# Kernel tuning notes

Hardware: AMD Instinct MI355X
Metric: run time of the kernel (lower is better)

Reference implementation:

```python
import jax, jax.numpy as jnp
import numpy as np

B = 65536      # batch size
H = 256        # hidden_size (args['hid_dim'])
MID = 300      # hard-coded encoder bottleneck in CommonFeatureExtractor
THR = 0.6      # similarity_threshold


def _lin(k, fin, fout):
    return jax.random.normal(k, (fin, fout), jnp.float32) / np.sqrt(fin)


def setup_inputs() -> dict:
    key = jax.random.key(0)
    ks = jax.random.split(key, 24)
    inp = {
        'brics': jax.random.normal(ks[0], (B, H), jnp.float32),
        'function_group': jax.random.normal(ks[1], (B, H), jnp.float32),
        'pharmacophore': jax.random.normal(ks[2], (B, H), jnp.float32),
    }
    # three fp encoders: Linear(H,300) -> ReLU -> (Dropout eval) -> Linear(300,H)
    for n, (k1, k2) in zip(['b', 'f', 'p'], [(ks[3], ks[4]), (ks[5], ks[6]), (ks[7], ks[8])]):
        inp['W1_' + n] = _lin(k1, H, MID)
        inp['b1_' + n] = jnp.zeros((MID,), jnp.float32)
        inp['W2_' + n] = _lin(k2, MID, H)
        inp['b2_' + n] = jnp.zeros((H,), jnp.float32)
    inp['Wg'] = _lin(ks[9], 3 * H, 3)        # weight_generator
    inp['bg_v'] = jnp.zeros((3,), jnp.float32)
    inp['We'] = _lin(ks[10], H, H)           # enhancement_layer
    inp['be_v'] = jnp.zeros((H,), jnp.float32)
    inp['Wf'] = _lin(ks[11], 2 * H, H)       # fusion_layer
    inp['bf_v'] = jnp.zeros((H,), jnp.float32)
    return inp


def _fwd(brics, function_group, pharmacophore,
         W1_b, b1_b, W2_b, b2_b, W1_f, b1_f, W2_f, b2_f, W1_p, b1_p, W2_p, b2_p,
         Wg, bg_v, We, be_v, Wf, bf_v):
    def enc(x, W1, b1, W2, b2):
        return jax.nn.relu(x @ W1 + b1) @ W2 + b2  # dropout in eval mode = identity

    eb = enc(brics, W1_b, b1_b, W2_b, b2_b)
    ef = enc(function_group, W1_f, b1_f, W2_f, b2_f)
    ep = enc(pharmacophore, W1_p, b1_p, W2_p, b2_p)

    fps = jnp.stack([eb, ef, ep], axis=1)                              # [B,3,H]
    fpn = fps / jnp.maximum(jnp.linalg.norm(fps, axis=-1, keepdims=True), 1e-12)

    # the 3 unordered pairs (0,1),(0,2),(1,2); the torch sort is irrelevant
    # because the selected pairs are combined by a permutation-invariant
    # softmax-weighted sum.
    ii = jnp.array([0, 0, 1])
    jj = jnp.array([1, 2, 2])
    elem = fpn[:, ii] * fpn[:, jj]                                     # [B,3,H]
    sims = elem.sum(-1)                                                # [B,3] cosine sims
    pmask = sims > THR
    common = 0.5 * (fps[:, ii] + fps[:, jj]) * (elem > THR)            # [B,3,H]

    has = pmask.any(-1)                                                # [B]
    m = jnp.max(jnp.where(pmask, sims, -jnp.inf), axis=-1, keepdims=True)
    m = jnp.where(jnp.isfinite(m), m, 0.0)
    e = jnp.where(pmask, jnp.exp(sims - m), 0.0)                       # masked softmax
    w = e / jnp.maximum(e.sum(-1, keepdims=True), 1e-12)
    sample_common = (common * w[..., None]).sum(1)                     # [B,H]
    common_features = jnp.where(has[:, None], sample_common, fps.mean(1))

    allc = jnp.concatenate([eb, ef, ep], axis=1)                       # [B,3H]
    fw = jax.nn.softmax(allc @ Wg + bg_v, axis=1)                      # [B,3]
    weighted = eb * fw[:, 0:1] + ef * fw[:, 1:2] + ep * fw[:, 2:3]

    enh = jax.nn.sigmoid(common_features @ We + be_v)
    fused = jnp.concatenate([weighted, common_features * enh], axis=1) @ Wf + bf_v
    return fused


def reference(brics, function_group, pharmacophore,
              W1_b, b1_b, W2_b, b2_b, W1_f, b1_f, W2_f, b2_f, W1_p, b1_p, W2_p, b2_p,
              Wg, bg_v, We, be_v, Wf, bf_v):
    return _fwd(brics, function_group, pharmacophore,
                W1_b, b1_b, W2_b, b2_b, W1_f, b1_f, W2_f, b2_f, W1_p, b1_p, W2_p, b2_p,
                Wg, bg_v, We, be_v, Wf, bf_v)
```

## Files before the change

### kernel.cpp

```cpp
#include <hip/hip_runtime.h>

typedef unsigned short u16;
typedef __bf16 bf16x8 __attribute__((ext_vector_type(8)));
typedef float f32x4 __attribute__((ext_vector_type(4)));
typedef unsigned short u16x8 __attribute__((ext_vector_type(8)));

__device__ __forceinline__ float b2f(u16 b){ union{unsigned u; float f;} v; v.u=((unsigned)b)<<16; return v.f; }
__device__ __forceinline__ u16 f2b(float f){ unsigned u=__builtin_bit_cast(unsigned,f); return (u16)((u+0x7fffu+((u>>16)&1u))>>16); }
__device__ __forceinline__ float wred32(float v){
  #pragma unroll
  for(int off=16; off>0; off>>=1) v += __shfl_xor(v, off, 64);
  return v;
}

__device__ __forceinline__ void gload_lds16(const void* g, void* l){
  __builtin_amdgcn_global_load_lds(
      (const __attribute__((address_space(1))) void*)g,
      (__attribute__((address_space(3))) void*)l, 16, 0, 0);
}

template<int PER>
__device__ __forceinline__ void stage_tile_b16(const u16* __restrict__ base, int rstride,
                                               int kcol, u16* lds, int w, int lane){
  #pragma unroll
  for(int it=0; it<PER; ++it){
    int cbase = it*512 + w*64;
    int ch = cbase + lane;
    int r = ch >> 3;
    int ce = ((ch & 7) * 8) ^ ((r & 7) << 3);
    gload_lds16(base + (size_t)r*rstride + kcol + ce, lds + cbase*8);
  }
}

struct Af32Regs { float4 a0, b0, a1, b1; };
__device__ __forceinline__ void loadA_f32(Af32Regs& rg, const float* __restrict__ Ap,
                                          int lda, int kcol, int tid){
  {
    int ch = tid;       int r = ch>>3, s = (ch&7)*8;
    const float* src = Ap + (size_t)r*lda + kcol + s;
    rg.a0 = *(const float4*)src; rg.b0 = *(const float4*)(src+4);
  }
  {
    int ch = tid + 512; int r = ch>>3, s = (ch&7)*8;
    const float* src = Ap + (size_t)r*lda + kcol + s;
    rg.a1 = *(const float4*)src; rg.b1 = *(const float4*)(src+4);
  }
}
__device__ __forceinline__ void writeA_f32(const Af32Regs& rg, u16* As, int tid){
  {
    int ch = tid;       int r = ch>>3, s = (ch&7)*8;
    u16* dst = &As[r*64 + (s ^ ((r&7)<<3))];
    ushort4 o0{f2b(rg.a0.x),f2b(rg.a0.y),f2b(rg.a0.z),f2b(rg.a0.w)};
    ushort4 o1{f2b(rg.b0.x),f2b(rg.b0.y),f2b(rg.b0.z),f2b(rg.b0.w)};
    *(ushort4*)dst = o0; *(ushort4*)(dst+4) = o1;
  }
  {
    int ch = tid + 512; int r = ch>>3, s = (ch&7)*8;
    u16* dst = &As[r*64 + (s ^ ((r&7)<<3))];
    ushort4 o0{f2b(rg.a1.x),f2b(rg.a1.y),f2b(rg.a1.z),f2b(rg.a1.w)};
    ushort4 o1{f2b(rg.b1.x),f2b(rg.b1.y),f2b(rg.b1.z),f2b(rg.b1.w)};
    *(ushort4*)dst = o0; *(ushort4*)(dst+4) = o1;
  }
}

struct GP {
  const void* A[3];
  const u16*  Wt[3];
  const float* bias[3];
  void* C[3];
  int lda, K, Nreal, ldc;
};

template<int MODE, typename AT, int NWT>
__global__ __launch_bounds__(512, 2) void gemm_w(GP p)
{
  constexpr int BN = NWT*64;
  constexpr int AHALF = 128*64;
  constexpr int BHALF = BN*64;
  __shared__ __align__(16) u16 smem[2*AHALF + 2*BHALF];

  const int z = blockIdx.z;
  const AT* __restrict__ A  = (const AT*)p.A[z];
  const u16* __restrict__ Wt = p.Wt[z];
  const float* __restrict__ bias = p.bias[z];
  u16* __restrict__ C = (u16*)p.C[z];
  const int lda = p.lda, K = p.K, ldc = p.ldc;

  const int tid = threadIdx.x;
  const size_t m0 = (size_t)blockIdx.x * 128;
  const int lane = tid & 63, w = tid >> 6;
  const int lr = lane & 15, quad = lane >> 4;
  const int wr = (w >> 2) * 64, wc = (w & 3) * (NWT*16);
  const int swz = (lr & 7) << 3;
  const int NT = K >> 6;

  f32x4 acc[4][NWT];
  #pragma unroll
  for(int i=0;i<4;++i)
    #pragma unroll
    for(int j=0;j<NWT;++j) acc[i][j] = (f32x4){0.f,0.f,0.f,0.f};

  const AT* Ab = A + m0*(size_t)lda;

  if constexpr (__is_same(AT, u16)) {
    stage_tile_b16<2>((const u16*)Ab, lda, 0, smem, w, lane);
  } else {
    Af32Regs rg; loadA_f32(rg, (const float*)Ab, lda, 0, tid);
    writeA_f32(rg, smem, tid);
  }
  stage_tile_b16<NWT>(Wt, K, 0, smem + 2*AHALF, w, lane);
  __syncthreads();

  int cur = 0;
  for(int t=0; t<NT; ++t){
    const int knext = (t+1) << 6;
    const bool pf = (t+1) < NT;
    Af32Regs rg;
    if (pf){
      if constexpr (__is_same(AT, u16))
        stage_tile_b16<2>((const u16*)Ab, lda, knext, smem + (cur^1)*AHALF, w, lane);
      else
        loadA_f32(rg, (const float*)Ab, lda, knext, tid);
      stage_tile_b16<NWT>(Wt, K, knext, smem + 2*AHALF + (cur^1)*BHALF, w, lane);
    }
    const u16* Asc = smem + cur*AHALF;
    const u16* Bsc = smem + 2*AHALF + cur*BHALF;
    #pragma unroll
    for(int kk=0; kk<64; kk+=32){
      bf16x8 af[4], bq[NWT];
      #pragma unroll
      for(int i=0;i<4;++i)
        af[i] = *(const bf16x8*)&Asc[(wr + i*16 + lr)*64 + ((kk + quad*8) ^ swz)];
      #pragma unroll
      for(int j=0;j<NWT;++j)
        bq[j] = *(const bf16x8*)&Bsc[(wc + j*16 + lr)*64 + ((kk + quad*8) ^ swz)];
      #pragma unroll
      for(int i=0;i<4;++i)
        #pragma unroll
        for(int j=0;j<NWT;++j)
          acc[i][j] = __builtin_amdgcn_mfma_f32_16x16x32_bf16(af[i], bq[j], acc[i][j], 0, 0, 0);
    }
    if constexpr (!__is_same(AT, u16)) { if (pf) writeA_f32(rg, smem + (cur^1)*AHALF, tid); }
    __syncthreads();
    cur ^= 1;
  }

  constexpr int BNP = BN + 8;
  static_assert(128*BNP <= 2*AHALF + 2*BHALF, "Ct fits in smem");
  u16* Ct = smem;
  #pragma unroll
  for(int j=0;j<NWT;++j){
    int col = wc + j*16 + lr;
    float bv = (col < p.Nreal) ? bias[col] : 0.f;
    #pragma unroll
    for(int i=0;i<4;++i){
      #pragma unroll
      for(int r=0;r<4;++r){
        float v = acc[i][j][r] + bv;
        if(MODE==1) v = fmaxf(v, 0.f);
        Ct[(wr + i*16 + quad*4 + r)*BNP + col] = f2b(v);
      }
    }
  }
  __syncthreads();
  const int rowg = tid >> 2, cg = tid & 3;
  const size_t crow = (m0 + rowg)*(size_t)ldc;
  #pragma unroll
  for(int k2=0; k2<BN/32; ++k2){
    int c = (cg + k2*4)*8;
    *(u16x8*)&C[crow + c] = *(const u16x8*)&Ct[rowg*BNP + c];
  }
}

struct TPar { const float* src; u16* dst; int K, N, Kp, Np; };
struct TArgs { TPar p[8]; };
__global__ __launch_bounds__(256) void transpose_all(TArgs args){
  TPar p = args.p[blockIdx.y];
  int n = blockIdx.x;
  if (n >= p.Np) return;
  for (int k = threadIdx.x; k < p.Kp; k += 256){
    u16 v = 0;
    if (n < p.N && k < p.K) v = f2b(p.src[(size_t)k*p.N + n]);
    p.dst[(size_t)n*p.Kp + k] = v;
  }
}

__global__ __launch_bounds__(512, 2) void fuse3_k(
    const u16* __restrict__ eb, const u16* __restrict__ ef, const u16* __restrict__ ep,
    const float* __restrict__ Wg, const float* __restrict__ bg,
    const u16* __restrict__ WtE, const float* __restrict__ be,
    const u16* __restrict__ WtF, const float* __restrict__ bfv,
    float* __restrict__ out)
{
  constexpr int BHALF = 256*64;
  __shared__ __align__(16) u16 cw[4*64*64];
  __shared__ __align__(16) u16 ww[4*64*64];
  __shared__ __align__(16) u16 Bst[2*BHALF];

  const int tid = threadIdx.x;
  const size_t m0 = (size_t)blockIdx.x * 64;
  const int lane = tid & 63, w = tid >> 6;
  const int lr = lane & 15, quad = lane >> 4;
  const int wr = (w >> 2) * 32, wc = (w & 3) * 64;
  const int swz = (lr & 7) << 3;

  stage_tile_b16<4>(WtE, 256, 0, Bst, w, lane);

  const int rid = tid >> 5, l5 = tid & 31;
  for(int pass=0; pass<4; ++pass){
    int rloc = pass*16 + rid;
    size_t base = (m0 + rloc)*256 + l5*8;

    u16x8 vb = *(const u16x8*)(eb + base);
    u16x8 vf = *(const u16x8*)(ef + base);
    u16x8 vp = *(const u16x8*)(ep + base);
    float fb[8], ff[8], fp[8];
    #pragma unroll
    for(int j=0;j<8;++j){ fb[j]=b2f(vb[j]); ff[j]=b2f(vf[j]); fp[j]=b2f(vp[j]); }

    float sb=0, sf=0, sp=0, d01=0, d02=0, d12=0, g0=0, g1=0, g2=0;
    #pragma unroll
    for(int j=0;j<8;++j){
      sb += fb[j]*fb[j]; sf += ff[j]*ff[j]; sp += fp[j]*fp[j];
      d01 += fb[j]*ff[j]; d02 += fb[j]*fp[j]; d12 += ff[j]*fp[j];
    }
    #pragma unroll
    for(int seg=0; seg<3; ++seg){
      const float* x = (seg==0) ? fb : (seg==1) ? ff : fp;
      const float* wg = Wg + ((size_t)seg*256 + l5*8)*3;
      float wv[24];
      #pragma unroll
      for(int q=0;q<6;++q){
        float4 t = *(const float4*)(wg + q*4);
        wv[q*4+0]=t.x; wv[q*4+1]=t.y; wv[q*4+2]=t.z; wv[q*4+3]=t.w;
      }
      #pragma unroll
      for(int j=0;j<8;++j){
        g0 += x[j]*wv[j*3+0];
        g1 += x[j]*wv[j*3+1];
        g2 += x[j]*wv[j*3+2];
      }
    }
    sb=wred32(sb); sf=wred32(sf); sp=wred32(sp);
    d01=wred32(d01); d02=wred32(d02); d12=wred32(d12);
    g0=wred32(g0); g1=wred32(g1); g2=wred32(g2);

    float inb  = __builtin_amdgcn_rsqf(fmaxf(sb, 1e-24f));
    float invf = __builtin_amdgcn_rsqf(fmaxf(sf, 1e-24f));
    float inp  = __builtin_amdgcn_rsqf(fmaxf(sp, 1e-24f));
    float s01 = d01*inb*invf, s02 = d02*inb*inp, s12 = d12*invf*inp;

    float h0 = g0 + bg[0], h1 = g1 + bg[1], h2 = g2 + bg[2];
    float gm = fmaxf(h0, fmaxf(h1, h2));
    float e0 = __expf(h0-gm), e1 = __expf(h1-gm), e2 = __expf(h2-gm);
    float res = __builtin_amdgcn_rcpf(e0+e1+e2);
    float fw0 = e0*res, fw1 = e1*res, fw2 = e2*res;

    bool p0 = s01 > 0.6f, p1 = s02 > 0.6f, p2 = s12 > 0.6f;
    bool has = p0 || p1 || p2;
    float mm = -__builtin_inff();
    if(p0) mm = fmaxf(mm, s01);
    if(p1) mm = fmaxf(mm, s02);
    if(p2) mm = fmaxf(mm, s12);
    if(!has) mm = 0.f;
    float q0 = p0 ? __expf(s01-mm) : 0.f;
    float q1 = p1 ? __expf(s02-mm) : 0.f;
    float q2 = p2 ? __expf(s12-mm) : 0.f;
    float rqs = __builtin_amdgcn_rcpf(fmaxf(q0+q1+q2, 1e-12f));
    float w0 = q0*rqs, w1 = q1*rqs, w2 = q2*rqs;

    u16x8 oc, ow;
    #pragma unroll
    for(int j=0;j<8;++j){
      float a = fb[j], b = ff[j], c = fp[j];
      float na = a*inb, nbv = b*invf, nc = c*inp;
      float c0 = (na*nbv > 0.6f) ? 0.5f*(a+b) : 0.f;
      float c1 = (na*nc  > 0.6f) ? 0.5f*(a+c) : 0.f;
      float c2 = (nbv*nc > 0.6f) ? 0.5f*(b+c) : 0.f;
      float sc = c0*w0 + c1*w1 + c2*w2;
      float cf = has ? sc : (a+b+c)*(1.f/3.f);
      float wv = a*fw0 + b*fw1 + c*fw2;
      oc[j] = f2b(cf); ow[j] = f2b(wv);
    }
    int idx = (l5>>3)*4096 + rloc*64 + (((l5&7)*8) ^ ((rloc&7)<<3));
    *(u16x8*)&cw[idx] = oc;
    *(u16x8*)&ww[idx] = ow;
  }
  __syncthreads();

  f32x4 ga[2][4];
  #pragma unroll
  for(int i=0;i<2;++i)
    #pragma unroll
    for(int j=0;j<4;++j) ga[i][j] = (f32x4){0.f,0.f,0.f,0.f};

  int cur = 0;
  for(int t=0; t<4; ++t){
    if(t<3) stage_tile_b16<4>(WtE, 256, (t+1)*64, Bst + (cur^1)*BHALF, w, lane);
    const u16* Asc = cw + t*4096;
    const u16* Bsc = Bst + cur*BHALF;
    #pragma unroll
    for(int kk=0; kk<64; kk+=32){
      bf16x8 af[2], bq[4];
      #pragma unroll
      for(int i=0;i<2;++i)
        af[i] = *(const bf16x8*)&Asc[(wr + i*16 + lr)*64 + ((kk + quad*8) ^ swz)];
      #pragma unroll
      for(int j=0;j<4;++j)
        bq[j] = *(const bf16x8*)&Bsc[(wc + j*16 + lr)*64 + ((kk + quad*8) ^ swz)];
      #pragma unroll
      for(int i=0;i<2;++i)
        #pragma unroll
        for(int j=0;j<4;++j)
          ga[i][j] = __builtin_amdgcn_mfma_f32_16x16x32_bf16(af[i], bq[j], ga[i][j], 0, 0, 0);
    }
    __syncthreads();
    cur ^= 1;
  }
  stage_tile_b16<4>(WtF, 512, 0, Bst, w, lane);

  #pragma unroll
  for(int j=0;j<4;++j){
    int col = wc + j*16 + lr;
    float bev = be[col];
    int within = j*16 + lr;
    #pragma unroll
    for(int i=0;i<2;++i){
      #pragma unroll
      for(int r=0;r<4;++r){
        int rl = wr + i*16 + quad*4 + r;
        int idx = (w & 3)*4096 + rl*64 + (within ^ ((rl&7)<<3));
        float cv = b2f(cw[idx]);
        float v = ga[i][j][r] + bev;
        cw[idx] = f2b(cv * __builtin_amdgcn_rcpf(1.f + __expf(-v)));
      }
    }
  }
  __syncthreads();

  f32x4 fa[2][4];
  #pragma unroll
  for(int i=0;i<2;++i)
    #pragma unroll
    for(int j=0;j<4;++j) fa[i][j] = (f32x4){0.f,0.f,0.f,0.f};

  cur = 0;
  for(int t=0; t<8; ++t){
    if(t<7) stage_tile_b16<4>(WtF, 512, (t+1)*64, Bst + (cur^1)*BHALF, w, lane);
    const u16* Asc = (t < 4) ? (ww + t*4096) : (cw + (t-4)*4096);
    const u16* Bsc = Bst + cur*BHALF;
    #pragma unroll
    for(int kk=0; kk<64; kk+=32){
      bf16x8 af[2], bq[4];
      #pragma unroll
      for(int i=0;i<2;++i)
        af[i] = *(const bf16x8*)&Asc[(wr + i*16 + lr)*64 + ((kk + quad*8) ^ swz)];
      #pragma unroll
      for(int j=0;j<4;++j)
        bq[j] = *(const bf16x8*)&Bsc[(wc + j*16 + lr)*64 + ((kk + quad*8) ^ swz)];
      #pragma unroll
      for(int i=0;i<2;++i)
        #pragma unroll
        for(int j=0;j<4;++j)
          fa[i][j] = __builtin_amdgcn_mfma_f32_16x16x32_bf16(af[i], bq[j], fa[i][j], 0, 0, 0);
    }
    __syncthreads();
    cur ^= 1;
  }

  #pragma unroll
  for(int j=0;j<4;++j){
    int col = wc + j*16 + lr;
    float bfc = bfv[col];
    #pragma unroll
    for(int i=0;i<2;++i){
      #pragma unroll
      for(int r=0;r<4;++r){
        size_t row = m0 + wr + i*16 + quad*4 + r;
        out[row*256 + col] = fa[i][j][r] + bfc;
      }
    }
  }
}

extern "C" void kernel_launch(void* const* d_in, const int* in_sizes, int n_in,
                              void* d_out, int out_size, void* d_ws, size_t ws_size,
                              hipStream_t stream) {
  const float* brics = (const float*)d_in[0];
  const float* fg    = (const float*)d_in[1];
  const float* ph    = (const float*)d_in[2];
  const float* W1[3] = {(const float*)d_in[3], (const float*)d_in[7], (const float*)d_in[11]};
  const float* b1[3] = {(const float*)d_in[4], (const float*)d_in[8], (const float*)d_in[12]};
  const float* W2[3] = {(const float*)d_in[5], (const float*)d_in[9], (const float*)d_in[13]};
  const float* b2[3] = {(const float*)d_in[6], (const float*)d_in[10], (const float*)d_in[14]};
  const float* Wg = (const float*)d_in[15];
  const float* bg = (const float*)d_in[16];
  const float* We = (const float*)d_in[17];
  const float* be = (const float*)d_in[18];
  const float* Wf = (const float*)d_in[19];
  const float* bf = (const float*)d_in[20];
  float* out = (float*)d_out;

  const int M = in_sizes[0] / 256;

  char* wsp = (char*)d_ws;
  size_t off = 0;
  auto carve = [&](size_t elems)->u16* {
    u16* p = (u16*)(wsp + off);
    off += ((elems*sizeof(u16)) + 255) & ~(size_t)255;
    return p;
  };
  u16* xb0 = carve((size_t)M*256);
  u16* xb1 = carve((size_t)M*256);
  u16* xb2 = carve((size_t)M*256);
  u16* Wt1[3], *Wt2[3];
  for(int i=0;i<3;++i) Wt1[i] = carve(320*256);
  for(int i=0;i<3;++i) Wt2[i] = carve(256*320);
  u16* WtE = carve(256*256);
  u16* WtF = carve(256*512);

  size_t hb = (((size_t)M*320*sizeof(u16)) + 255) & ~(size_t)255;
  bool batched = (off + 3*hb) <= ws_size;
  u16* hh[3];
  hh[0] = (u16*)(wsp + off);
  hh[1] = batched ? (u16*)(wsp + off + hb)   : hh[0];
  hh[2] = batched ? (u16*)(wsp + off + 2*hb) : hh[0];
  (void)n_in; (void)out_size;

  TArgs ta;
  for(int i=0;i<3;++i){
    ta.p[i]   = {W1[i], Wt1[i], 256, 300, 256, 320};
    ta.p[3+i] = {W2[i], Wt2[i], 300, 256, 320, 256};
  }
  ta.p[6] = {We, WtE, 256, 256, 256, 256};
  ta.p[7] = {Wf, WtF, 512, 256, 512, 256};
  transpose_all<<<dim3(512, 8), 256, 0, stream>>>(ta);

  const float* xin[3] = {brics, fg, ph};
  u16* encp[3] = {xb0, xb1, xb2};
  if (batched) {
    GP g1{};
    for(int i=0;i<3;++i){ g1.A[i]=xin[i]; g1.Wt[i]=Wt1[i]; g1.bias[i]=b1[i]; g1.C[i]=hh[i]; }
    g1.lda=256; g1.K=256; g1.Nreal=300; g1.ldc=320;
    gemm_w<1,float,5><<<dim3(M/128, 1, 3), 512, 0, stream>>>(g1);
    GP g2{};
    for(int i=0;i<3;++i){ g2.A[i]=hh[i]; g2.Wt[i]=Wt2[i]; g2.bias[i]=b2[i]; g2.C[i]=encp[i]; }
    g2.lda=320; g2.K=320; g2.Nreal=256; g2.ldc=256;
    gemm_w<0,u16,4><<<dim3(M/128, 1, 3), 512, 0, stream>>>(g2);
  } else {
    for(int i=0;i<3;++i){
      GP g1{}; g1.A[0]=xin[i]; g1.Wt[0]=Wt1[i]; g1.bias[0]=b1[i]; g1.C[0]=hh[0];
      g1.lda=256; g1.K=256; g1.Nreal=300; g1.ldc=320;
      gemm_w<1,float,5><<<dim3(M/128, 1, 1), 512, 0, stream>>>(g1);
      GP g2{}; g2.A[0]=hh[0]; g2.Wt[0]=Wt2[i]; g2.bias[0]=b2[i]; g2.C[0]=encp[i];
      g2.lda=320; g2.K=320; g2.Nreal=256; g2.ldc=256;
      gemm_w<0,u16,4><<<dim3(M/128, 1, 1), 512, 0, stream>>>(g2);
    }
  }

  fuse3_k<<<M/64, 512, 0, stream>>>(xb0, xb1, xb2, Wg, bg, WtE, be, WtF, bf, out);
}
```

Measured before the change: 434.4 us.

## Fuse both encoder GEMMs into one kernel and read weights directly from global

Replaces the two batched encoder GEMM launches with a single kernel that keeps the 64x320 ReLU hidden tile in LDS and feeds it straight into the second GEMM. This removes the round trip of the M x 320 bf16 intermediate through global memory and one launch. The weight operands, in both the encoder and the fusion kernel, are now loaded straight from global into registers instead of being staged through double-buffered LDS, and fuse3_k's occupancy hint is raised. The cost is uncoalesced-ish per-lane weight loads relying on cache, and no software pipelining of A loads.

```diff
diff --git a/kernel.cpp b/kernel.cpp
--- a/kernel.cpp
+++ b/kernel.cpp
@@ -12,163 +12,122 @@
   for(int off=16; off>0; off>>=1) v += __shfl_xor(v, off, 64);
   return v;
 }
-
-__device__ __forceinline__ void gload_lds16(const void* g, void* l){
-  __builtin_amdgcn_global_load_lds(
-      (const __attribute__((address_space(1))) void*)g,
-      (__attribute__((address_space(3))) void*)l, 16, 0, 0);
-}
-
-template<int PER>
-__device__ __forceinline__ void stage_tile_b16(const u16* __restrict__ base, int rstride,
-                                               int kcol, u16* lds, int w, int lane){
-  #pragma unroll
-  for(int it=0; it<PER; ++it){
-    int cbase = it*512 + w*64;
-    int ch = cbase + lane;
-    int r = ch >> 3;
-    int ce = ((ch & 7) * 8) ^ ((r & 7) << 3);
-    gload_lds16(base + (size_t)r*rstride + kcol + ce, lds + cbase*8);
-  }
-}
-
-struct Af32Regs { float4 a0, b0, a1, b1; };
-__device__ __forceinline__ void loadA_f32(Af32Regs& rg, const float* __restrict__ Ap,
-                                          int lda, int kcol, int tid){
-  {
-    int ch = tid;       int r = ch>>3, s = (ch&7)*8;
-    const float* src = Ap + (size_t)r*lda + kcol + s;
-    rg.a0 = *(const float4*)src; rg.b0 = *(const float4*)(src+4);
-  }
-  {
-    int ch = tid + 512; int r = ch>>3, s = (ch&7)*8;
-    const float* src = Ap + (size_t)r*lda + kcol + s;
-    rg.a1 = *(const float4*)src; rg.b1 = *(const float4*)(src+4);
-  }
-}
-__device__ __forceinline__ void writeA_f32(const Af32Regs& rg, u16* As, int tid){
-  {
-    int ch = tid;       int r = ch>>3, s = (ch&7)*8;
-    u16* dst = &As[r*64 + (s ^ ((r&7)<<3))];
-    ushort4 o0{f2b(rg.a0.x),f2b(rg.a0.y),f2b(rg.a0.z),f2b(rg.a0.w)};
-    ushort4 o1{f2b(rg.b0.x),f2b(rg.b0.y),f2b(rg.b0.z),f2b(rg.b0.w)};
-    *(ushort4*)dst = o0; *(ushort4*)(dst+4) = o1;
-  }
-  {
-    int ch = tid + 512; int r = ch>>3, s = (ch&7)*8;
-    u16* dst = &As[r*64 + (s ^ ((r&7)<<3))];
-    ushort4 o0{f2b(rg.a1.x),f2b(rg.a1.y),f2b(rg.a1.z),f2b(rg.a1.w)};
-    ushort4 o1{f2b(rg.b1.x),f2b(rg.b1.y),f2b(rg.b1.z),f2b(rg.b1.w)};
-    *(ushort4*)dst = o0; *(ushort4*)(dst+4) = o1;
-  }
-}
-
-struct GP {
-  const void* A[3];
-  const u16*  Wt[3];
-  const float* bias[3];
-  void* C[3];
-  int lda, K, Nreal, ldc;
+__device__ __forceinline__ bf16x8 cvt8(float4 lo, float4 hi){
+  u16x8 t;
+  t[0]=f2b(lo.x); t[1]=f2b(lo.y); t[2]=f2b(lo.z); t[3]=f2b(lo.w);
+  t[4]=f2b(hi.x); t[5]=f2b(hi.y); t[6]=f2b(hi.z); t[7]=f2b(hi.w);
+  return __builtin_bit_cast(bf16x8, t);
+}
+
+struct EP {
+  const float* X[3];
+  const u16*  W1[3];
+  const float* B1[3];
+  const u16*  W2[3];
+  const float* B2[3];
+  u16* E[3];
 };
 
-template<int MODE, typename AT, int NWT>
-__global__ __launch_bounds__(512, 2) void gemm_w(GP p)
+__global__ __launch_bounds__(256, 3) void enc_k(EP p)
 {
-  constexpr int BN = NWT*64;
-  constexpr int AHALF = 128*64;
-  constexpr int BHALF = BN*64;
-  __shared__ __align__(16) u16 smem[2*AHALF + 2*BHALF];
-
+  constexpr int CH = 4096;
+  __shared__ __align__(16) u16 hs[5*CH];
   const int z = blockIdx.z;
-  const AT* __restrict__ A  = (const AT*)p.A[z];
-  const u16* __restrict__ Wt = p.Wt[z];
-  const float* __restrict__ bias = p.bias[z];
-  u16* __restrict__ C = (u16*)p.C[z];
-  const int lda = p.lda, K = p.K, ldc = p.ldc;
+  const float* __restrict__ X   = p.X[z];
+  const u16*   __restrict__ W1  = p.W1[z];
+  const float* __restrict__ b1v = p.B1[z];
+  const u16*   __restrict__ W2  = p.W2[z];
+  const float* __restrict__ b2v = p.B2[z];
+  u16* __restrict__ E = p.E[z];
 
   const int tid = threadIdx.x;
-  const size_t m0 = (size_t)blockIdx.x * 128;
+  const size_t m0 = (size_t)blockIdx.x * 64;
   const int lane = tid & 63, w = tid >> 6;
   const int lr = lane & 15, quad = lane >> 4;
-  const int wr = (w >> 2) * 64, wc = (w & 3) * (NWT*16);
   const int swz = (lr & 7) << 3;
-  const int NT = K >> 6;
-
-  f32x4 acc[4][NWT];
+
+  const int wc1 = w * 80;
+  f32x4 acc1[4][5];
   #pragma unroll
   for(int i=0;i<4;++i)
     #pragma unroll
-    for(int j=0;j<NWT;++j) acc[i][j] = (f32x4){0.f,0.f,0.f,0.f};
-
-  const AT* Ab = A + m0*(size_t)lda;
-
-  if constexpr (__is_same(AT, u16)) {
-    stage_tile_b16<2>((const u16*)Ab, lda, 0, smem, w, lane);
-  } else {
-    Af32Regs rg; loadA_f32(rg, (const float*)Ab, lda, 0, tid);
-    writeA_f32(rg, smem, tid);
-  }
-  stage_tile_b16<NWT>(Wt, K, 0, smem + 2*AHALF, w, lane);
-  __syncthreads();
-
-  int cur = 0;
-  for(int t=0; t<NT; ++t){
-    const int knext = (t+1) << 6;
-    const bool pf = (t+1) < NT;
-    Af32Regs rg;
-    if (pf){
-      if constexpr (__is_same(AT, u16))
-        stage_tile_b16<2>((const u16*)Ab, lda, knext, smem + (cur^1)*AHALF, w, lane);
-      else
-        loadA_f32(rg, (const float*)Ab, lda, knext, tid);
-      stage_tile_b16<NWT>(Wt, K, knext, smem + 2*AHALF + (cur^1)*BHALF, w, lane);
-    }
-    const u16* Asc = smem + cur*AHALF;
-    const u16* Bsc = smem + 2*AHALF + cur*BHALF;
-    #pragma unroll
-    for(int kk=0; kk<64; kk+=32){
-      bf16x8 af[4], bq[NWT];
-      #pragma unroll
-      for(int i=0;i<4;++i)
-        af[i] = *(const bf16x8*)&Asc[(wr + i*16 + lr)*64 + ((kk + quad*8) ^ swz)];
-      #pragma unroll
-      for(int j=0;j<NWT;++j)
-        bq[j] = *(const bf16x8*)&Bsc[(wc + j*16 + lr)*64 + ((kk + quad*8) ^ swz)];
-      #pragma unroll
-      for(int i=0;i<4;++i)
-        #pragma unroll
-        for(int j=0;j<NWT;++j)
-          acc[i][j] = __builtin_amdgcn_mfma_f32_16x16x32_bf16(af[i], bq[j], acc[i][j], 0, 0, 0);
-    }
-    if constexpr (!__is_same(AT, u16)) { if (pf) writeA_f32(rg, smem + (cur^1)*AHALF, tid); }
-    __syncthreads();
-    cur ^= 1;
-  }
-
-  constexpr int BNP = BN + 8;
-  static_assert(128*BNP <= 2*AHALF + 2*BHALF, "Ct fits in smem");
-  u16* Ct = smem;
-  #pragma unroll
-  for(int j=0;j<NWT;++j){
-    int col = wc + j*16 + lr;
-    float bv = (col < p.Nreal) ? bias[col] : 0.f;
+    for(int j=0;j<5;++j) acc1[i][j] = (f32x4){0.f,0.f,0.f,0.f};
+
+  const float* Xb = X + m0*256;
+  for(int kk=0; kk<256; kk+=32){
+    bf16x8 afr[4], bfr[5];
     #pragma unroll
     for(int i=0;i<4;++i){
+      const float* s = Xb + (size_t)(i*16+lr)*256 + kk + quad*8;
+      float4 lo = *(const float4*)s, hi = *(const float4*)(s+4);
+      afr[i] = cvt8(lo, hi);
+    }
+    #pragma unroll
+    for(int j=0;j<5;++j)
+      bfr[j] = *(const bf16x8*)&W1[(size_t)(wc1+j*16+lr)*256 + kk + quad*8];
+    #pragma unroll
+    for(int i=0;i<4;++i)
+      #pragma unroll
+      for(int j=0;j<5;++j)
+        acc1[i][j] = __builtin_amdgcn_mfma_f32_16x16x32_bf16(afr[i], bfr[j], acc1[i][j], 0, 0, 0);
+  }
+  #pragma unroll
+  for(int j=0;j<5;++j){
+    int col = wc1 + j*16 + lr;
+    float bv = (col < 300) ? b1v[col] : 0.f;
+    int c = col >> 6, cwi = col & 63;
+    #pragma unroll
+    for(int i=0;i<4;++i)
       #pragma unroll
       for(int r=0;r<4;++r){
-        float v = acc[i][j][r] + bv;
-        if(MODE==1) v = fmaxf(v, 0.f);
-        Ct[(wr + i*16 + quad*4 + r)*BNP + col] = f2b(v);
-      }
-    }
+        int row = i*16 + quad*4 + r;
+        float v = fmaxf(acc1[i][j][r] + bv, 0.f);
+        hs[c*CH + row*64 + (cwi ^ ((row&7)<<3))] = f2b(v);
+      }
+  }
+  __syncthreads();
+
+  const int wc2 = w * 64;
+  f32x4 acc2[4][4];
+  #pragma unroll
+  for(int i=0;i<4;++i)
+    #pragma unroll
+    for(int j=0;j<4;++j) acc2[i][j] = (f32x4){0.f,0.f,0.f,0.f};
+
+  for(int kkg=0; kkg<320; kkg+=32){
+    const int c = kkg >> 6, kk = kkg & 63;
+    bf16x8 afr[4], bfr[4];
+    #pragma unroll
+    for(int i=0;i<4;++i)
+      afr[i] = *(const bf16x8*)&hs[c*CH + (i*16+lr)*64 + ((kk + quad*8) ^ swz)];
+    #pragma unroll
+    for(int j=0;j<4;++j)
+      bfr[j] = *(const bf16x8*)&W2[(size_t)(wc2+j*16+lr)*320 + kkg + quad*8];
+    #pragma unroll
+    for(int i=0;i<4;++i)
+      #pragma unroll
+      for(int j=0;j<4;++j)
+        acc2[i][j] = __builtin_amdgcn_mfma_f32_16x16x32_bf16(afr[i], bfr[j], acc2[i][j], 0, 0, 0);
+  }
+  __syncthreads();
+  u16* Ct = hs;
+  #pragma unroll
+  for(int j=0;j<4;++j){
+    int col = wc2 + j*16 + lr;
+    float bv = b2v[col];
+    #pragma unroll
+    for(int i=0;i<4;++i)
+      #pragma unroll
+      for(int r=0;r<4;++r)
+        Ct[(i*16 + quad*4 + r)*264 + col] = f2b(acc2[i][j][r] + bv);
   }
   __syncthreads();
   const int rowg = tid >> 2, cg = tid & 3;
-  const size_t crow = (m0 + rowg)*(size_t)ldc;
-  #pragma unroll
-  for(int k2=0; k2<BN/32; ++k2){
-    int c = (cg + k2*4)*8;
-    *(u16x8*)&C[crow + c] = *(const u16x8*)&Ct[rowg*BNP + c];
+  const size_t crow = (m0 + rowg)*256;
+  #pragma unroll
+  for(int k2=0; k2<8; ++k2){
+    int cc = (cg + k2*4)*8;
+    *(u16x8*)&E[crow + cc] = *(const u16x8*)&Ct[rowg*264 + cc];
   }
 }
 
@@ -185,17 +144,15 @@
   }
 }
 
-__global__ __launch_bounds__(512, 2) void fuse3_k(
+__global__ __launch_bounds__(512, 4) void fuse3_k(
     const u16* __restrict__ eb, const u16* __restrict__ ef, const u16* __restrict__ ep,
     const float* __restrict__ Wg, const float* __restrict__ bg,
     const u16* __restrict__ WtE, const float* __restrict__ be,
     const u16* __restrict__ WtF, const float* __restrict__ bfv,
     float* __restrict__ out)
 {
-  constexpr int BHALF = 256*64;
-  __shared__ __align__(16) u16 cw[4*64*64];
-  __shared__ __align__(16) u16 ww[4*64*64];
-  __shared__ __align__(16) u16 Bst[2*BHALF];
+  __shared__ __align__(16) u16 cw[4*4096];
+  __shared__ __align__(16) u16 ww[4*4096];
 
   const int tid = threadIdx.x;
   const size_t m0 = (size_t)blockIdx.x * 64;
@@ -203,8 +160,6 @@
   const int lr = lane & 15, quad = lane >> 4;
   const int wr = (w >> 2) * 32, wc = (w & 3) * 64;
   const int swz = (lr & 7) << 3;
-
-  stage_tile_b16<4>(WtE, 256, 0, Bst, w, lane);
 
   const int rid = tid >> 5, l5 = tid & 31;
   for(int pass=0; pass<4; ++pass){
@@ -294,30 +249,22 @@
     #pragma unroll
     for(int j=0;j<4;++j) ga[i][j] = (f32x4){0.f,0.f,0.f,0.f};
 
-  int cur = 0;
-  for(int t=0; t<4; ++t){
-    if(t<3) stage_tile_b16<4>(WtE, 256, (t+1)*64, Bst + (cur^1)*BHALF, w, lane);
-    const u16* Asc = cw + t*4096;
-    const u16* Bsc = Bst + cur*BHALF;
-    #pragma unroll
-    for(int kk=0; kk<64; kk+=32){
-      bf16x8 af[2], bq[4];
-      #pragma unroll
-      for(int i=0;i<2;++i)
-        af[i] = *(const bf16x8*)&Asc[(wr + i*16 + lr)*64 + ((kk + quad*8) ^ swz)];
+  for(int kkg=0; kkg<256; kkg+=32){
+    const int c = kkg >> 6, kk = kkg & 63;
+    bf16x8 af[2], bq[4];
+    #pragma unroll
+    for(int i=0;i<2;++i)
+      af[i] = *(const bf16x8*)&cw[c*4096 + (wr+i*16+lr)*64 + ((kk + quad*8) ^ swz)];
+    #pragma unroll
+    for(int j=0;j<4;++j)
+      bq[j] = *(const bf16x8*)&WtE[(size_t)(wc+j*16+lr)*256 + kkg + quad*8];
+    #pragma unroll
+    for(int i=0;i<2;++i)
       #pragma unroll
       for(int j=0;j<4;++j)
-        bq[j] = *(const bf16x8*)&Bsc[(wc + j*16 + lr)*64 + ((kk + quad*8) ^ swz)];
-      #pragma unroll
-      for(int i=0;i<2;++i)
-        #pragma unroll
-        for(int j=0;j<4;++j)
-          ga[i][j] = __builtin_amdgcn_mfma_f32_16x16x32_bf16(af[i], bq[j], ga[i][j], 0, 0, 0);
-    }
-    __syncthreads();
-    cur ^= 1;
-  }
-  stage_tile_b16<4>(WtF, 512, 0, Bst, w, lane);
+        ga[i][j] = __builtin_amdgcn_mfma_f32_16x16x32_bf16(af[i], bq[j], ga[i][j], 0, 0, 0);
+  }
+  __syncthreads();
 
   #pragma unroll
   for(int j=0;j<4;++j){
@@ -344,28 +291,21 @@
     #pragma unroll
     for(int j=0;j<4;++j) fa[i][j] = (f32x4){0.f,0.f,0.f,0.f};
 
-  cur = 0;
-  for(int t=0; t<8; ++t){
-    if(t<7) stage_tile_b16<4>(WtF, 512, (t+1)*64, Bst + (cur^1)*BHALF, w, lane);
+  for(int kkg=0; kkg<512; kkg+=32){
+    const int t = kkg >> 6, kk = kkg & 63;
     const u16* Asc = (t < 4) ? (ww + t*4096) : (cw + (t-4)*4096);
-    const u16* Bsc = Bst + cur*BHALF;
-    #pragma unroll
-    for(int kk=0; kk<64; kk+=32){
-      bf16x8 af[2], bq[4];
-      #pragma unroll
-      for(int i=0;i<2;++i)
-        af[i] = *(const bf16x8*)&Asc[(wr + i*16 + lr)*64 + ((kk + quad*8) ^ swz)];
+    bf16x8 af[2], bq[4];
+    #pragma unroll
+    for(int i=0;i<2;++i)
+      af[i] = *(const bf16x8*)&Asc[(wr+i*16+lr)*64 + ((kk + quad*8) ^ swz)];
+    #pragma unroll
+    for(int j=0;j<4;++j)
+      bq[j] = *(const bf16x8*)&WtF[(size_t)(wc+j*16+lr)*512 + kkg + quad*8];
+    #pragma unroll
+    for(int i=0;i<2;++i)
       #pragma unroll
       for(int j=0;j<4;++j)
-        bq[j] = *(const bf16x8*)&Bsc[(wc + j*16 + lr)*64 + ((kk + quad*8) ^ swz)];
-      #pragma unroll
-      for(int i=0;i<2;++i)
-        #pragma unroll
-        for(int j=0;j<4;++j)
-          fa[i][j] = __builtin_amdgcn_mfma_f32_16x16x32_bf16(af[i], bq[j], fa[i][j], 0, 0, 0);
-    }
-    __syncthreads();
-    cur ^= 1;
+        fa[i][j] = __builtin_amdgcn_mfma_f32_16x16x32_bf16(af[i], bq[j], fa[i][j], 0, 0, 0);
   }
 
   #pragma unroll
@@ -418,14 +358,7 @@
   for(int i=0;i<3;++i) Wt2[i] = carve(256*320);
   u16* WtE = carve(256*256);
   u16* WtF = carve(256*512);
-
-  size_t hb = (((size_t)M*320*sizeof(u16)) + 255) & ~(size_t)255;
-  bool batched = (off + 3*hb) <= ws_size;
-  u16* hh[3];
-  hh[0] = (u16*)(wsp + off);
-  hh[1] = batched ? (u16*)(wsp + off + hb)   : hh[0];
-  hh[2] = batched ? (u16*)(wsp + off + 2*hb) : hh[0];
-  (void)n_in; (void)out_size;
+  (void)n_in; (void)out_size; (void)ws_size;
 
   TArgs ta;
   for(int i=0;i<3;++i){
@@ -436,27 +369,14 @@
   ta.p[7] = {Wf, WtF, 512, 256, 512, 256};
   transpose_all<<<dim3(512, 8), 256, 0, stream>>>(ta);
 
+  EP ep_{};
   const float* xin[3] = {brics, fg, ph};
   u16* encp[3] = {xb0, xb1, xb2};
-  if (batched) {
-    GP g1{};
-    for(int i=0;i<3;++i){ g1.A[i]=xin[i]; g1.Wt[i]=Wt1[i]; g1.bias[i]=b1[i]; g1.C[i]=hh[i]; }
-    g1.lda=256; g1.K=256; g1.Nreal=300; g1.ldc=320;
-    gemm_w<1,float,5><<<dim3(M/128, 1, 3), 512, 0, stream>>>(g1);
-    GP g2{};
-    for(int i=0;i<3;++i){ g2.A[i]=hh[i]; g2.Wt[i]=Wt2[i]; g2.bias[i]=b2[i]; g2.C[i]=encp[i]; }
-    g2.lda=320; g2.K=320; g2.Nreal=256; g2.ldc=256;
-    gemm_w<0,u16,4><<<dim3(M/128, 1, 3), 512, 0, stream>>>(g2);
-  } else {
-    for(int i=0;i<3;++i){
-      GP g1{}; g1.A[0]=xin[i]; g1.Wt[0]=Wt1[i]; g1.bias[0]=b1[i]; g1.C[0]=hh[0];
-      g1.lda=256; g1.K=256; g1.Nreal=300; g1.ldc=320;
-      gemm_w<1,float,5><<<dim3(M/128, 1, 1), 512, 0, stream>>>(g1);
-      GP g2{}; g2.A[0]=hh[0]; g2.Wt[0]=Wt2[i]; g2.bias[0]=b2[i]; g2.C[0]=encp[i];
-      g2.lda=320; g2.K=320; g2.Nreal=256; g2.ldc=256;
-      gemm_w<0,u16,4><<<dim3(M/128, 1, 1), 512, 0, stream>>>(g2);
-    }
-  }
+  for(int i=0;i<3;++i){
+    ep_.X[i]=xin[i]; ep_.W1[i]=Wt1[i]; ep_.B1[i]=b1[i];
+    ep_.W2[i]=Wt2[i]; ep_.B2[i]=b2[i]; ep_.E[i]=encp[i];
+  }
+  enc_k<<<dim3(M/64, 1, 3), 256, 0, stream>>>(ep_);
 
   fuse3_k<<<M/64, 512, 0, stream>>>(xb0, xb1, xb2, Wg, bg, WtE, be, WtF, bf, out);
 }
```

Measured after the change: 551.8 us. 27.0% more time.
